# Performance work log

Measured on AMD Instinct MI355X. Metric: run time of the kernel, lower is better.

The kernel has to match this reference:

```python
import jax, jax.numpy as jnp
import numpy as np

S = 16          # state_dim
H = 96          # hidden_dim
A = 64          # num_actions
B = 256         # batch_size
D_IN = S * S * 64      # 16384
D_H = H * H            # 9216
SPLIT = D_H - S * S    # 8960, action/selection split point


def setup_inputs() -> dict:
    key = jax.random.key(0)
    ks = jax.random.split(key, 14)
    s = jax.random.normal(ks[0], (B, S, S, 64), dtype=jnp.float32)
    mask = jax.random.randint(ks[1], (B, S, S), 0, 2).astype(bool)
    u = jax.random.uniform(ks[2], (B, S * S), dtype=jnp.float32,
                           minval=1e-6, maxval=1.0 - 1e-6)
    def lin(k, fin, fout):
        kw, kb = jax.random.split(k)
        sc = 1.0 / np.sqrt(fin)
        return (jax.random.uniform(kw, (fin, fout), minval=-sc, maxval=sc, dtype=jnp.float32),
                jax.random.uniform(kb, (fout,), minval=-sc, maxval=sc, dtype=jnp.float32))
    W1, b1 = lin(ks[3], D_IN, D_H)
    W2, b2 = lin(ks[4], D_H, D_H)
    W3, b3 = lin(ks[5], D_H, D_H)
    Wa, ba = lin(ks[6], SPLIT, A)
    Ws, bs = lin(ks[7], S * S, S * S)
    return {"s": s, "mask": mask, "u": u, "W1": W1, "b1": b1, "W2": W2,
            "b2": b2, "W3": W3, "b3": b3, "Wa": Wa, "ba": ba, "Ws": Ws, "bs": bs}


def reference(s, mask, u, W1, b1, W2, b2, W3, b3, Wa, ba, Ws, bs):
    x = s.reshape(s.shape[0], -1).astype(jnp.float32)        # [B, D_IN]
    x = jax.nn.relu(x @ W1 + b1)                             # [B, D_H]
    x = jax.nn.relu(x @ W2 + b2)
    x = jax.nn.relu(x @ W3 + b3)
    x_action = jax.nn.softmax(x[:, :SPLIT] @ Wa + ba, axis=1)  # [B, A]
    # selection branch
    p = jax.nn.softmax(x[:, SPLIT:] @ Ws + bs, axis=1)         # [B, S*S]
    m = mask.reshape(mask.shape[0], -1)                        # [B, S*S]
    p = jnp.where(m, -1e9, p)        # masked_fill on the probs (faithful)
    p = jax.nn.softmax(p, axis=1)
    # parallel Gumbel-max == Categorical over valid (unnormalized) probs
    gumbel = -jnp.log(-jnp.log(u))
    scores = jnp.where(m, -jnp.inf, jnp.log(p) + gumbel)
    idx = jnp.argmax(scores, axis=1)                           # [B]
    coordinate = jnp.stack([idx // S, idx % S], axis=1)        # [B, 2]
    sel_prob = jnp.take_along_axis(p, idx[:, None], axis=1)    # [B, 1]
    final_action_prob = x_action * sel_prob                    # [B, A]
    return final_action_prob, coordinate
```

## Files before the change

### kernel.cpp

```cpp
#include <hip/hip_runtime.h>
#include <hip/hip_fp16.h>


typedef _Float16 f16;
typedef _Float16 f16x4 __attribute__((ext_vector_type(4)));
typedef _Float16 f16x8 __attribute__((ext_vector_type(8)));
typedef float f32x4 __attribute__((ext_vector_type(4)));

#define DH 9216
#define SPLIT 8960

__device__ __forceinline__ void gload16(const void* g, void* l) {
    __builtin_amdgcn_global_load_lds(
        (const __attribute__((address_space(1))) void*)g,
        (__attribute__((address_space(3))) void*)l, 16, 0, 0);
}

__global__ void cvt_kernel(const float* __restrict__ in, f16* __restrict__ out, int n) {
    for (int i = (blockIdx.x * blockDim.x + threadIdx.x) * 4; i < n;
         i += gridDim.x * blockDim.x * 4) {
        float4 v = *(const float4*)(in + i);
        f16x4 h = {(_Float16)v.x, (_Float16)v.y, (_Float16)v.z, (_Float16)v.w};
        *(f16x4*)(out + i) = h;
    }
}

__global__ __launch_bounds__(256, 3) void gemm_kernel(
    const f16* __restrict__ A, int K, int Kh, int yshift,
    const float* __restrict__ W,
    f16* __restrict__ P)
{
    __shared__ __align__(16) char lds[2][24576];
    const int bid  = blockIdx.x;
    const int y    = bid & ((1 << yshift) - 1);
    const int rem  = bid >> yshift;
    const int m0   = (rem & 1) << 7;
    const int n0   = (rem >> 1) << 7;
    const int tid  = threadIdx.x;
    const int lane = tid & 63;
    const int wid  = tid >> 6;
    const int wm   = wid >> 1, wn = wid & 1;
    const int kbase = y * Kh;
    const int ns   = Kh >> 5;

    f32x4 acc[4][4] = {};

    const float* wsrc0;
    const float* wsrc1;
    const float* wsrc2;
    const float* wsrc3;
    {
        int g0 = tid,      k0 = g0 >> 5, c0 = (g0 & 31) ^ ((5 * (k0 >> 3)) & 31);
        int g1 = tid + 256, k1 = g1 >> 5, c1 = (g1 & 31) ^ ((5 * (k1 >> 3)) & 31);
        int g2 = tid + 512, k2 = g2 >> 5, c2 = (g2 & 31) ^ ((5 * (k2 >> 3)) & 31);
        int g3 = tid + 768, k3 = g3 >> 5, c3 = (g3 & 31) ^ ((5 * (k3 >> 3)) & 31);
        wsrc0 = W + (size_t)(kbase + k0) * DH + n0 + (c0 << 2);
        wsrc1 = W + (size_t)(kbase + k1) * DH + n0 + (c1 << 2);
        wsrc2 = W + (size_t)(kbase + k2) * DH + n0 + (c2 << 2);
        wsrc3 = W + (size_t)(kbase + k3) * DH + n0 + (c3 << 2);
    }
    const f16* asrc0;
    const f16* asrc1;
    {
        int h0 = tid, h1 = tid + 256;
        int r0 = m0 + ((h0 >> 8) << 6) + (((h0 >> 6) & 3) << 4) + (h0 & 15);
        int r1 = m0 + ((h1 >> 8) << 6) + (((h1 >> 6) & 3) << 4) + (h1 & 15);
        asrc0 = A + (size_t)r0 * K + kbase + (((h0 >> 4) & 3) << 3);
        asrc1 = A + (size_t)r1 * K + kbase + (((h1 >> 4) & 3) << 3);
    }

    auto issue = [&](int slot) {
        char* dst = &lds[slot][0];
        gload16(wsrc0, dst + (size_t)tid * 16);          wsrc0 += 32 * DH;
        gload16(wsrc1, dst + (size_t)(tid + 256) * 16);  wsrc1 += 32 * DH;
        gload16(wsrc2, dst + (size_t)(tid + 512) * 16);  wsrc2 += 32 * DH;
        gload16(wsrc3, dst + (size_t)(tid + 768) * 16);  wsrc3 += 32 * DH;
        gload16(asrc0, dst + 16384 + (size_t)tid * 16);         asrc0 += 32;
        gload16(asrc1, dst + 16384 + (size_t)(tid + 256) * 16); asrc1 += 32;
    };

    const int q  = lane >> 4;
    const int lc = lane & 15;
    auto step = [&](int slot) {
        const float* wl = (const float*)&lds[slot][0];
        const f16*   al = (const f16*)&lds[slot][16384];
        f16x8 af[4], bf[4];
#pragma unroll
        for (int ri = 0; ri < 4; ++ri)
            af[ri] = *(const f16x8*)(al + (((wm << 8) + (ri << 6) + lane) << 3));
        const int wbase = (q << 10) + (lc & 3);
#pragma unroll
        for (int ni = 0; ni < 4; ++ni) {
            int p = ((wn << 4) + (ni << 2) + (lc >> 2)) ^ (5 * q);
            int fi = wbase + ((p & 31) << 2);
            f16x8 b;
#pragma unroll
            for (int j = 0; j < 8; ++j)
                b[j] = (_Float16)wl[fi + (j << 7)];
            bf[ni] = b;
        }
#pragma unroll
        for (int ri = 0; ri < 4; ++ri)
#pragma unroll
            for (int ni = 0; ni < 4; ++ni)
                acc[ri][ni] = __builtin_amdgcn_mfma_f32_16x16x32_f16(
                    af[ri], bf[ni], acc[ri][ni], 0, 0, 0);
    };

    issue(0);
    issue(1);
    __builtin_amdgcn_sched_barrier(0);

    for (int t = 0; t < ns; ++t) {
        if (t + 1 < ns) asm volatile("s_waitcnt vmcnt(6)" ::: "memory");
        else            asm volatile("s_waitcnt vmcnt(0)" ::: "memory");
        __builtin_amdgcn_sched_barrier(0);
        __builtin_amdgcn_s_barrier();
        __builtin_amdgcn_sched_barrier(0);
        step(t & 1);
        __builtin_amdgcn_sched_barrier(0);
        asm volatile("s_waitcnt lgkmcnt(0)" ::: "memory");
        __builtin_amdgcn_sched_barrier(0);
        __builtin_amdgcn_s_barrier();
        __builtin_amdgcn_sched_barrier(0);
        if (t + 2 < ns) {
            issue(t & 1);
            __builtin_amdgcn_sched_barrier(0);
        }
    }

    f16* Pb = P + (size_t)y * (256 * DH);
#pragma unroll
    for (int ri = 0; ri < 4; ++ri) {
        int row = m0 + wm * 64 + ri * 16 + (q << 2);
#pragma unroll
        for (int ni = 0; ni < 4; ++ni) {
            int col = n0 + wn * 64 + ni * 16 + lc;
#pragma unroll
            for (int rg = 0; rg < 4; ++rg)
                Pb[(size_t)(row + rg) * DH + col] = (_Float16)acc[ri][ni][rg];
        }
    }
}

__global__ __launch_bounds__(256) void reduce_kernel(
    const f16* __restrict__ P, int S,
    const float* __restrict__ bias,
    f16* __restrict__ oh, float* __restrict__ out32) {
    const size_t n = 256 * DH;
    const size_t i = ((size_t)blockIdx.x * 256 + threadIdx.x) * 8;
    if (i >= n) return;
    float r[8];
    {
        float4 b0 = *(const float4*)(bias + (i % DH));
        float4 b1 = *(const float4*)(bias + (i % DH) + 4);
        r[0] = b0.x; r[1] = b0.y; r[2] = b0.z; r[3] = b0.w;
        r[4] = b1.x; r[5] = b1.y; r[6] = b1.z; r[7] = b1.w;
    }
    for (int j = 0; j < S; ++j) {
        f16x8 v = *(const f16x8*)(P + (size_t)j * n + i);
#pragma unroll
        for (int e = 0; e < 8; ++e) r[e] += (float)v[e];
    }
#pragma unroll
    for (int e = 0; e < 8; ++e) r[e] = fmaxf(r[e], 0.f);
    if (oh) {
        f16x8 h;
#pragma unroll
        for (int e = 0; e < 8; ++e) h[e] = (_Float16)r[e];
        *(f16x8*)(oh + i) = h;
    }
    if (out32) {
        float4 o0 = {r[0], r[1], r[2], r[3]};
        float4 o1 = {r[4], r[5], r[6], r[7]};
        *(float4*)(out32 + i) = o0;
        *(float4*)(out32 + i + 4) = o1;
    }
}

__global__ __launch_bounds__(256) void action_kernel(
    const float* __restrict__ X3, const float* __restrict__ Wa,
    const float* __restrict__ ba, float* __restrict__ xact) {
    __shared__ float xs[SPLIT];
    __shared__ float red[256];
    const int row = blockIdx.x, t = threadIdx.x;
    const float* xr = X3 + (size_t)row * DH;
    for (int k = t * 4; k < SPLIT; k += 1024)
        *(float4*)&xs[k] = *(const float4*)(xr + k);
    __syncthreads();
    const int col = t & 63, kqq = t >> 6;
    float acc = 0.f;
    for (int k = kqq * 2240; k < (kqq + 1) * 2240; ++k)
        acc += xs[k] * Wa[(size_t)k * 64 + col];
    red[t] = acc;
    __syncthreads();
    if (t < 64) {
        float z = red[t] + red[t + 64] + red[t + 128] + red[t + 192] + ba[t];
        float mx = z;
        for (int off = 32; off; off >>= 1) mx = fmaxf(mx, __shfl_xor(mx, off));
        float e = expf(z - mx);
        float s = e;
        for (int off = 32; off; off >>= 1) s += __shfl_xor(s, off);
        xact[row * 64 + t] = e / s;
    }
}

__global__ __launch_bounds__(256) void select_kernel(
    const float* __restrict__ X3, const float* __restrict__ Ws,
    const float* __restrict__ bs, const void* __restrict__ maskp,
    const float* __restrict__ u, const float* __restrict__ xact,
    float* __restrict__ out) {
    __shared__ float xs[256];
    __shared__ float psh[256];
    __shared__ float rr[4];
    __shared__ float bestv[4];
    __shared__ int besti[4];
    __shared__ int sIdx;
    __shared__ int smode;
    const int row = blockIdx.x, t = threadIdx.x;
    const int lane = t & 63, wid = t >> 6;

    if (t < 64) {
        unsigned v = ((const unsigned*)maskp)[t];
        int okInt  = __all(v <= 1u);
        int okByte = __all((v & 0xFEFEFEFEu) == 0u);
        if (t == 0) smode = okInt ? 0 : (okByte ? 1 : 2);
    }
    xs[t] = X3[(size_t)row * DH + SPLIT + t];
    __syncthreads();

    bool mk;
    if (smode == 0)       mk = ((const int*)maskp)[row * 256 + t] != 0;
    else if (smode == 1)  mk = ((const unsigned char*)maskp)[row * 256 + t] != 0;
    else                  mk = ((const float*)maskp)[row * 256 + t] != 0.0f;

    float z = bs[t];
    for (int k = 0; k < 256; ++k)
        z += xs[k] * Ws[k * 256 + t];

    float v = z;
    for (int off = 32; off; off >>= 1) v = fmaxf(v, __shfl_xor(v, off));
    if (lane == 0) rr[wid] = v;
    __syncthreads();
    float m1 = fmaxf(fmaxf(rr[0], rr[1]), fmaxf(rr[2], rr[3]));
    __syncthreads();
    float e1 = expf(z - m1);
    v = e1;
    for (int off = 32; off; off >>= 1) v += __shfl_xor(v, off);
    if (lane == 0) rr[wid] = v;
    __syncthreads();
    float s1 = rr[0] + rr[1] + rr[2] + rr[3];
    __syncthreads();
    float p1 = e1 / s1;

    float q = mk ? -1e9f : p1;
    v = q;
    for (int off = 32; off; off >>= 1) v = fmaxf(v, __shfl_xor(v, off));
    if (lane == 0) rr[wid] = v;
    __syncthreads();
    float m2 = fmaxf(fmaxf(rr[0], rr[1]), fmaxf(rr[2], rr[3]));
    __syncthreads();
    float e2 = expf(q - m2);
    v = e2;
    for (int off = 32; off; off >>= 1) v += __shfl_xor(v, off);
    if (lane == 0) rr[wid] = v;
    __syncthreads();
    float s2 = rr[0] + rr[1] + rr[2] + rr[3];
    float p2 = e2 / s2;
    psh[t] = p2;

    float g = -logf(-logf(u[row * 256 + t]));
    float sc = mk ? -INFINITY : (logf(p2) + g);
    float bv = sc;
    int bi = t;
    for (int off = 32; off; off >>= 1) {
        float ov = __shfl_xor(bv, off);
        int oi = __shfl_xor(bi, off);
        if (ov > bv || (ov == bv && oi < bi)) { bv = ov; bi = oi; }
    }
    if (lane == 0) { bestv[wid] = bv; besti[wid] = bi; }
    __syncthreads();
    if (t == 0) {
        float fv = bestv[0];
        int fi = besti[0];
        for (int w = 1; w < 4; ++w)
            if (bestv[w] > fv || (bestv[w] == fv && besti[w] < fi)) {
                fv = bestv[w]; fi = besti[w];
            }
        sIdx = fi;
    }
    __syncthreads();
    const int idx = sIdx;
    const float sp = psh[idx];
    if (t < 64) out[row * 64 + t] = xact[row * 64 + t] * sp;
    if (t == 0) {
        out[256 * 64 + row * 2 + 0] = (float)(idx >> 4);
        out[256 * 64 + row * 2 + 1] = (float)(idx & 15);
    }
}

extern "C" void kernel_launch(void* const* d_in, const int* in_sizes, int n_in,
                              void* d_out, int out_size, void* d_ws, size_t ws_size,
                              hipStream_t stream) {
    const float* s  = (const float*)d_in[0];
    const void*  mask = d_in[1];
    const float* u  = (const float*)d_in[2];
    const float* W1 = (const float*)d_in[3];
    const float* b1 = (const float*)d_in[4];
    const float* W2 = (const float*)d_in[5];
    const float* b2 = (const float*)d_in[6];
    const float* W3 = (const float*)d_in[7];
    const float* b3 = (const float*)d_in[8];
    const float* Wa = (const float*)d_in[9];
    const float* ba = (const float*)d_in[10];
    const float* Ws = (const float*)d_in[11];
    const float* bs = (const float*)d_in[12];
    float* out = (float*)d_out;
    char* ws = (char*)d_ws;

    f16*   A0 = (f16*)(ws + 0);
    f16*   X1 = (f16*)(ws + 8388608);
    f16*   X2 = (f16*)(ws + 0);
    float* X3 = (float*)(ws + 13107200);
    float* XA = (float*)(ws + 22544384);
    f16*   P  = (f16*)(ws + 22609920);

    const size_t pbytes = 4718592ull;
    int yshift = (ws_size >= 22609920ull + 8 * pbytes) ? 3 : 2;
    const int S = 1 << yshift;

    cvt_kernel<<<2048, 256, 0, stream>>>(s, A0, 256 * 16384);

    const int nblk = (2 * 72) << yshift;
    gemm_kernel<<<nblk, 256, 0, stream>>>(A0, 16384, 16384 / S, yshift, W1, P);
    reduce_kernel<<<1152, 256, 0, stream>>>(P, S, b1, X1, nullptr);
    gemm_kernel<<<nblk, 256, 0, stream>>>(X1, DH, DH / S, yshift, W2, P);
    reduce_kernel<<<1152, 256, 0, stream>>>(P, S, b2, X2, nullptr);
    gemm_kernel<<<nblk, 256, 0, stream>>>(X2, DH, DH / S, yshift, W3, P);
    reduce_kernel<<<1152, 256, 0, stream>>>(P, S, b3, nullptr, X3);

    action_kernel<<<256, 256, 0, stream>>>(X3, Wa, ba, XA);
    select_kernel<<<256, 256, 0, stream>>>(X3, Ws, bs, mask, u, XA, out);
}
```

Measured before the change: 561.2 us.

## Load A fragments directly to registers and triple-buffer W tiles in LDS

The GEMM kernel stops staging the fp16 activation tile through LDS. Each wave now loads its A fragments straight from global memory into registers, double-buffered as even and odd sets. The fp32 weight tiles move to a three-slot LDS ring, so two tiles are in flight while one is consumed. The main loop is unrolled by two, with hand-tuned vmcnt waits. This aims to hide more weight-load latency and cut LDS traffic for A, at the cost of more VGPRs, uncoalesced per-lane A loads, and fragile waitcnt accounting.

```diff
diff --git a/kernel.cpp b/kernel.cpp
--- a/kernel.cpp
+++ b/kernel.cpp
@@ -30,7 +30,7 @@
     const float* __restrict__ W,
     f16* __restrict__ P)
 {
-    __shared__ __align__(16) char lds[2][24576];
+    __shared__ __align__(16) char lds[3][16384];
     const int bid  = blockIdx.x;
     const int y    = bid & ((1 << yshift) - 1);
     const int rem  = bid >> yshift;
@@ -44,6 +44,7 @@
     const int ns   = Kh >> 5;
 
     f32x4 acc[4][4] = {};
+    f16x8 aE[4], aO[4];
 
     const float* wsrc0;
     const float* wsrc1;
@@ -59,36 +60,26 @@
         wsrc2 = W + (size_t)(kbase + k2) * DH + n0 + (c2 << 2);
         wsrc3 = W + (size_t)(kbase + k3) * DH + n0 + (c3 << 2);
     }
-    const f16* asrc0;
-    const f16* asrc1;
-    {
-        int h0 = tid, h1 = tid + 256;
-        int r0 = m0 + ((h0 >> 8) << 6) + (((h0 >> 6) & 3) << 4) + (h0 & 15);
-        int r1 = m0 + ((h1 >> 8) << 6) + (((h1 >> 6) & 3) << 4) + (h1 & 15);
-        asrc0 = A + (size_t)r0 * K + kbase + (((h0 >> 4) & 3) << 3);
-        asrc1 = A + (size_t)r1 * K + kbase + (((h1 >> 4) & 3) << 3);
-    }
-
-    auto issue = [&](int slot) {
-        char* dst = &lds[slot][0];
+    const int q  = lane >> 4;
+    const int lc = lane & 15;
+    const f16* abase = A + (size_t)(m0 + wm * 64 + lc) * K + kbase + (q << 3);
+
+    auto issueW = [&](char* dst) {
         gload16(wsrc0, dst + (size_t)tid * 16);          wsrc0 += 32 * DH;
         gload16(wsrc1, dst + (size_t)(tid + 256) * 16);  wsrc1 += 32 * DH;
         gload16(wsrc2, dst + (size_t)(tid + 512) * 16);  wsrc2 += 32 * DH;
         gload16(wsrc3, dst + (size_t)(tid + 768) * 16);  wsrc3 += 32 * DH;
-        gload16(asrc0, dst + 16384 + (size_t)tid * 16);         asrc0 += 32;
-        gload16(asrc1, dst + 16384 + (size_t)(tid + 256) * 16); asrc1 += 32;
     };
-
-    const int q  = lane >> 4;
-    const int lc = lane & 15;
-    auto step = [&](int slot) {
-        const float* wl = (const float*)&lds[slot][0];
-        const f16*   al = (const f16*)&lds[slot][16384];
-        f16x8 af[4], bf[4];
+    auto loadA = [&](f16x8* a, int t) {
+        const f16* p = abase + (t << 5);
 #pragma unroll
         for (int ri = 0; ri < 4; ++ri)
-            af[ri] = *(const f16x8*)(al + (((wm << 8) + (ri << 6) + lane) << 3));
+            a[ri] = *(const f16x8*)(p + (size_t)(ri << 4) * K);
+    };
+    auto step = [&](const char* wslotp, f16x8* a) {
+        const float* wl = (const float*)wslotp;
         const int wbase = (q << 10) + (lc & 3);
+        f16x8 bf[4];
 #pragma unroll
         for (int ni = 0; ni < 4; ++ni) {
             int p = ((wn << 4) + (ni << 2) + (lc >> 2)) ^ (5 * q);
@@ -104,29 +95,57 @@
 #pragma unroll
             for (int ni = 0; ni < 4; ++ni)
                 acc[ri][ni] = __builtin_amdgcn_mfma_f32_16x16x32_f16(
-                    af[ri], bf[ni], acc[ri][ni], 0, 0, 0);
+                    a[ri], bf[ni], acc[ri][ni], 0, 0, 0);
     };
 
-    issue(0);
-    issue(1);
+    loadA(aE, 0);
+    issueW(&lds[0][0]);
+    loadA(aO, 1);
+    issueW(&lds[1][0]);
+    issueW(&lds[2][0]);
     __builtin_amdgcn_sched_barrier(0);
 
-    for (int t = 0; t < ns; ++t) {
-        if (t + 1 < ns) asm volatile("s_waitcnt vmcnt(6)" ::: "memory");
-        else            asm volatile("s_waitcnt vmcnt(0)" ::: "memory");
+    int wslot = 0;
+    for (int t = 0; t < ns; t += 2) {
+        if (t < ns - 2)       asm volatile("s_waitcnt vmcnt(12)" ::: "memory");
+        else if (t == ns - 2) asm volatile("s_waitcnt vmcnt(8)"  ::: "memory");
+        else                  asm volatile("s_waitcnt vmcnt(0)"  ::: "memory");
         __builtin_amdgcn_sched_barrier(0);
         __builtin_amdgcn_s_barrier();
         __builtin_amdgcn_sched_barrier(0);
-        step(t & 1);
-        __builtin_amdgcn_sched_barrier(0);
-        asm volatile("s_waitcnt lgkmcnt(0)" ::: "memory");
+        {
+            char* wp = &lds[wslot][0];
+            step(wp, aE);
+            __builtin_amdgcn_sched_barrier(0);
+            asm volatile("s_waitcnt lgkmcnt(0)" ::: "memory");
+            __builtin_amdgcn_sched_barrier(0);
+            __builtin_amdgcn_s_barrier();
+            __builtin_amdgcn_sched_barrier(0);
+            if (t + 2 < ns) loadA(aE, t + 2);
+            if (t + 3 < ns) issueW(wp);
+            __builtin_amdgcn_sched_barrier(0);
+        }
+        wslot = (wslot == 2) ? 0 : wslot + 1;
+
+        if (t + 1 < ns - 2)       asm volatile("s_waitcnt vmcnt(12)" ::: "memory");
+        else if (t + 1 == ns - 2) asm volatile("s_waitcnt vmcnt(8)"  ::: "memory");
+        else                      asm volatile("s_waitcnt vmcnt(0)"  ::: "memory");
         __builtin_amdgcn_sched_barrier(0);
         __builtin_amdgcn_s_barrier();
         __builtin_amdgcn_sched_barrier(0);
-        if (t + 2 < ns) {
-            issue(t & 1);
+        {
+            char* wp = &lds[wslot][0];
+            step(wp, aO);
+            __builtin_amdgcn_sched_barrier(0);
+            asm volatile("s_waitcnt lgkmcnt(0)" ::: "memory");
+            __builtin_amdgcn_sched_barrier(0);
+            __builtin_amdgcn_s_barrier();
+            __builtin_amdgcn_sched_barrier(0);
+            if (t + 3 < ns) loadA(aO, t + 3);
+            if (t + 4 < ns) issueW(wp);
             __builtin_amdgcn_sched_barrier(0);
         }
+        wslot = (wslot == 2) ? 0 : wslot + 1;
     }
 
     f16* Pb = P + (size_t)y * (256 * DH);
```

Measured after the change: 644.1 us. 14.8% more time.

## Pre-pack activations into tile-contiguous layout for GEMM A-operand loads

Applied to the files above, without the earlier changes.

The fp16 activation matrices are now written by the convert and reduce kernels directly in the per-tile order the GEMM stages into LDS. Each 32-wide K step of a 128-row tile becomes one contiguous 8 KB chunk, so the GEMM's A loads turn from strided row reads into sequential 16-byte reads. The cost is scattered writes in the producer kernels. The change is meant to improve coalescing and cut address arithmetic in the weight-bound GEMM, where A traffic is a small share of the total.

```diff
diff --git a/kernel.cpp b/kernel.cpp
--- a/kernel.cpp
+++ b/kernel.cpp
@@ -16,17 +16,26 @@
         (__attribute__((address_space(3))) void*)l, 16, 0, 0);
 }
 
-__global__ void cvt_kernel(const float* __restrict__ in, f16* __restrict__ out, int n) {
-    for (int i = (blockIdx.x * blockDim.x + threadIdx.x) * 4; i < n;
-         i += gridDim.x * blockDim.x * 4) {
-        float4 v = *(const float4*)(in + i);
-        f16x4 h = {(_Float16)v.x, (_Float16)v.y, (_Float16)v.z, (_Float16)v.w};
-        *(f16x4*)(out + i) = h;
-    }
+__device__ __forceinline__ size_t pk_off(int row, int k) {
+    int tk = k >> 5, q = (k >> 3) & 3;
+    int mhalf = row >> 7, wmA = (row >> 6) & 1, ri = (row >> 4) & 3, lc = row & 15;
+    int h = (wmA << 8) | (ri << 6) | (q << 4) | lc;
+    return (size_t)(tk * 2 + mhalf) * 8192 + (size_t)h * 16;
+}
+
+__global__ void cvt_kernel(const float* __restrict__ in, char* __restrict__ outp) {
+    int idx = blockIdx.x * blockDim.x + threadIdx.x;
+    int row = idx >> 11;
+    int k8  = (idx & 2047) << 3;
+    const float* src = in + ((size_t)row << 14) + k8;
+    f16x8 h;
+#pragma unroll
+    for (int j = 0; j < 8; ++j) h[j] = (_Float16)src[j];
+    *(f16x8*)(outp + pk_off(row, k8)) = h;
 }
 
 __global__ __launch_bounds__(256, 3) void gemm_kernel(
-    const f16* __restrict__ A, int K, int Kh, int yshift,
+    const char* __restrict__ Ap, int K, int Kh, int yshift,
     const float* __restrict__ W,
     f16* __restrict__ P)
 {
@@ -59,15 +68,7 @@
         wsrc2 = W + (size_t)(kbase + k2) * DH + n0 + (c2 << 2);
         wsrc3 = W + (size_t)(kbase + k3) * DH + n0 + (c3 << 2);
     }
-    const f16* asrc0;
-    const f16* asrc1;
-    {
-        int h0 = tid, h1 = tid + 256;
-        int r0 = m0 + ((h0 >> 8) << 6) + (((h0 >> 6) & 3) << 4) + (h0 & 15);
-        int r1 = m0 + ((h1 >> 8) << 6) + (((h1 >> 6) & 3) << 4) + (h1 & 15);
-        asrc0 = A + (size_t)r0 * K + kbase + (((h0 >> 4) & 3) << 3);
-        asrc1 = A + (size_t)r1 * K + kbase + (((h1 >> 4) & 3) << 3);
-    }
+    const char* ap = Ap + (size_t)(y * (Kh >> 5) * 2 + (m0 >> 7)) * 8192;
 
     auto issue = [&](int slot) {
         char* dst = &lds[slot][0];
@@ -75,8 +76,9 @@
         gload16(wsrc1, dst + (size_t)(tid + 256) * 16);  wsrc1 += 32 * DH;
         gload16(wsrc2, dst + (size_t)(tid + 512) * 16);  wsrc2 += 32 * DH;
         gload16(wsrc3, dst + (size_t)(tid + 768) * 16);  wsrc3 += 32 * DH;
-        gload16(asrc0, dst + 16384 + (size_t)tid * 16);         asrc0 += 32;
-        gload16(asrc1, dst + 16384 + (size_t)(tid + 256) * 16); asrc1 += 32;
+        gload16(ap + (size_t)tid * 16,        dst + 16384 + (size_t)tid * 16);
+        gload16(ap + (size_t)tid * 16 + 4096, dst + 16384 + (size_t)tid * 16 + 4096);
+        ap += 16384;
     };
 
     const int q  = lane >> 4;
@@ -146,14 +148,16 @@
 __global__ __launch_bounds__(256) void reduce_kernel(
     const f16* __restrict__ P, int S,
     const float* __restrict__ bias,
-    f16* __restrict__ oh, float* __restrict__ out32) {
+    char* __restrict__ ohp, float* __restrict__ out32) {
     const size_t n = 256 * DH;
     const size_t i = ((size_t)blockIdx.x * 256 + threadIdx.x) * 8;
     if (i >= n) return;
+    const int row = (int)(i / DH);
+    const int d   = (int)(i % DH);
     float r[8];
     {
-        float4 b0 = *(const float4*)(bias + (i % DH));
-        float4 b1 = *(const float4*)(bias + (i % DH) + 4);
+        float4 b0 = *(const float4*)(bias + d);
+        float4 b1 = *(const float4*)(bias + d + 4);
         r[0] = b0.x; r[1] = b0.y; r[2] = b0.z; r[3] = b0.w;
         r[4] = b1.x; r[5] = b1.y; r[6] = b1.z; r[7] = b1.w;
     }
@@ -164,11 +168,11 @@
     }
 #pragma unroll
     for (int e = 0; e < 8; ++e) r[e] = fmaxf(r[e], 0.f);
-    if (oh) {
+    if (ohp) {
         f16x8 h;
 #pragma unroll
         for (int e = 0; e < 8; ++e) h[e] = (_Float16)r[e];
-        *(f16x8*)(oh + i) = h;
+        *(f16x8*)(ohp + pk_off(row, d)) = h;
     }
     if (out32) {
         float4 o0 = {r[0], r[1], r[2], r[3]};
@@ -318,25 +322,25 @@
     float* out = (float*)d_out;
     char* ws = (char*)d_ws;
 
-    f16*   A0 = (f16*)(ws + 0);
-    f16*   X1 = (f16*)(ws + 8388608);
-    f16*   X2 = (f16*)(ws + 0);
-    float* X3 = (float*)(ws + 13107200);
-    float* XA = (float*)(ws + 22544384);
-    f16*   P  = (f16*)(ws + 22609920);
+    char*  A0p = ws + 0;
+    char*  X1p = ws + 8388608;
+    char*  X2p = ws + 0;
+    float* X3  = (float*)(ws + 13107200);
+    float* XA  = (float*)(ws + 22544384);
+    f16*   P   = (f16*)(ws + 22609920);
 
     const size_t pbytes = 4718592ull;
     int yshift = (ws_size >= 22609920ull + 8 * pbytes) ? 3 : 2;
     const int S = 1 << yshift;
 
-    cvt_kernel<<<2048, 256, 0, stream>>>(s, A0, 256 * 16384);
+    cvt_kernel<<<2048, 256, 0, stream>>>(s, A0p);
 
     const int nblk = (2 * 72) << yshift;
-    gemm_kernel<<<nblk, 256, 0, stream>>>(A0, 16384, 16384 / S, yshift, W1, P);
-    reduce_kernel<<<1152, 256, 0, stream>>>(P, S, b1, X1, nullptr);
-    gemm_kernel<<<nblk, 256, 0, stream>>>(X1, DH, DH / S, yshift, W2, P);
-    reduce_kernel<<<1152, 256, 0, stream>>>(P, S, b2, X2, nullptr);
-    gemm_kernel<<<nblk, 256, 0, stream>>>(X2, DH, DH / S, yshift, W3, P);
+    gemm_kernel<<<nblk, 256, 0, stream>>>(A0p, 16384, 16384 / S, yshift, W1, P);
+    reduce_kernel<<<1152, 256, 0, stream>>>(P, S, b1, X1p, nullptr);
+    gemm_kernel<<<nblk, 256, 0, stream>>>(X1p, DH, DH / S, yshift, W2, P);
+    reduce_kernel<<<1152, 256, 0, stream>>>(P, S, b2, X2p, nullptr);
+    gemm_kernel<<<nblk, 256, 0, stream>>>(X2p, DH, DH / S, yshift, W3, P);
     reduce_kernel<<<1152, 256, 0, stream>>>(P, S, b3, nullptr, X3);
 
     action_kernel<<<256, 256, 0, stream>>>(X3, Wa, ba, XA);
```

Result: faster. 514.4 us (-8.4%).
